# Optimization experiments

Hardware: AMD Instinct MI355X
Metric: run time of the kernel (lower is better)

## Reference

```python
import jax, jax.numpy as jnp
import numpy as np

EPS = 1e-5  # torch BatchNorm default eps


def _bn(x, gamma, beta, axes):
    # training-mode batch norm over `axes`, channel dim is axis 1
    mean = jnp.mean(x, axis=axes, keepdims=True)
    var = jnp.var(x, axis=axes, keepdims=True)
    shape = [1] * x.ndim
    shape[1] = -1
    return (x - mean) * jax.lax.rsqrt(var + EPS) * gamma.reshape(shape) + beta.reshape(shape)


def setup_inputs() -> dict:
    B, C, N = 16, 512, 192
    S_RATIO, R_RATIO = 4, 8
    Cs, Cr = C // S_RATIO, C // R_RATIO  # 128, 64
    inter = N * Cr + C  # 12800
    key = jax.random.key(0)
    ks = jax.random.split(key, 6)

    def w(k, shp, fan):
        return jax.random.normal(k, shp, jnp.float32) * np.float32(np.sqrt(2.0 / fan))

    return {
        "inputs": jax.random.normal(ks[0], (B, C, N), jnp.float32),
        "retain": 0,
        "theta_w": w(ks[1], (Cs, C), Cs), "theta_b": jnp.zeros((Cs,), jnp.float32),
        "theta_g": jnp.ones((Cs,), jnp.float32), "theta_be": jnp.zeros((Cs,), jnp.float32),
        "phi_w": w(ks[2], (Cs, C), Cs), "phi_b": jnp.zeros((Cs,), jnp.float32),
        "phi_g": jnp.ones((Cs,), jnp.float32), "phi_be": jnp.zeros((Cs,), jnp.float32),
        "re_w": w(ks[3], (Cr, Cs), Cr), "re_b": jnp.zeros((Cr,), jnp.float32),
        "re_g": jnp.ones((Cr,), jnp.float32), "re_be": jnp.zeros((Cr,), jnp.float32),
        "att_w": w(ks[4], (C, inter), C), "att_b": jnp.zeros((C,), jnp.float32),
        "att_g": jnp.ones((C,), jnp.float32), "att_be": jnp.zeros((C,), jnp.float32),
    }


def reference(inputs, retain, theta_w, theta_b, theta_g, theta_be,
              phi_w, phi_b, phi_g, phi_be, re_w, re_b, re_g, re_be,
              att_w, att_b, att_g, att_be):
    B, C, N = inputs.shape
    xt = inputs.transpose(0, 2, 1)  # [B, N, C]

    # theta / phi pro_blocks: Linear -> BN1d (over B,N) -> ReLU, output [B, Cs, N]
    th = jax.nn.relu(_bn(jnp.einsum('bnc,oc->bon', xt, theta_w) + theta_b[None, :, None], theta_g, theta_be, (0, 2)))
    ph = jax.nn.relu(_bn(jnp.einsum('bnc,oc->bon', xt, phi_w) + phi_b[None, :, None], phi_g, phi_be, (0, 2)))
    th = th.transpose(0, 2, 1)  # [B, N, Cs]
    ph = ph.transpose(0, 2, 1)  # [B, N, Cs]

    # pairwise broadcast-diff: [B, N, N, Cs]
    diff = th[:, :, None, :] - ph[:, None, :, :]

    # pro_block1: Linear -> BN2d -> ReLU, then flatten to [B, N, N*Cr]
    rel = jnp.einsum('bijc,oc->boij', diff, re_w) + re_b[None, :, None, None]  # [B, Cr, N, N]
    rel = jax.nn.relu(_bn(rel, re_g, re_be, (0, 2, 3)))
    rel = rel.transpose(0, 2, 3, 1).reshape(B, N, -1)  # [B, N, N*Cr]

    # attention_generator: Linear -> BN1d -> sigmoid, output [B, C, N]
    cat = jnp.concatenate([xt, rel], axis=2)  # [B, N, C + N*Cr]
    att = jnp.einsum('bni,oi->bon', cat, att_w) + att_b[None, :, None]  # [B, C, N]
    att = jax.nn.sigmoid(_bn(att, att_g, att_be, (0, 2)))

    features = att * inputs  # [B, C, N]
    if retain:
        return features
    return jnp.sum(features, axis=2) / jnp.sum(att, axis=2)  # [B, C]
```

## Files before the change

kernel.cpp:

```cpp
#include <hip/hip_runtime.h>

#define BB 16
#define CC 512
#define NN 192
#define CS 128
#define CR 64
#define EPSF 1e-5f
#define PART (BB*CC*NN)

typedef __attribute__((ext_vector_type(8))) short short8;
typedef __attribute__((ext_vector_type(4))) float f32x4;
typedef __attribute__((ext_vector_type(4))) unsigned int uint4v;

#define OFF_LIN2  0
#define OFF_P2    786432
#define OFF_QT    983040
#define OFF_ATTP4 1179648
#define OFF_WBF   7471104
#define OFF_XT    10747904
#define OFF_ROWS  11534336
#define OFF_SPART 11567104

__device__ __forceinline__ unsigned pkbf(float a, float b){
  unsigned r; asm("v_cvt_pk_bf16_f32 %0, %1, %2" : "=v"(r) : "v"(a), "v"(b)); return r;
}

__device__ __forceinline__ void gload_lds16(const void* g, void* l){
  __builtin_amdgcn_global_load_lds(
      (const __attribute__((address_space(1))) unsigned int*)g,
      (__attribute__((address_space(3))) unsigned int*)l, 16, 0, 0);
}

__global__ __launch_bounds__(256) void kconvxt(
    const float* __restrict__ aw, const float* __restrict__ x,
    short* __restrict__ wbf, short* __restrict__ xT)
{
  __shared__ float Ts[64][65];
  if (blockIdx.x < 3200) {
    int t = blockIdx.x*256 + threadIdx.x;
    int o2 = t / 1600;
    int kk = (t - o2*1600) * 8;
    const float* src = &aw[o2*12800 + kk];
    float4 v0 = *reinterpret_cast<const float4*>(src);
    float4 v1 = *reinterpret_cast<const float4*>(src+4);
    uint4v w;
    w.x = pkbf(v0.x, v0.y); w.y = pkbf(v0.z, v0.w);
    w.z = pkbf(v1.x, v1.y); w.w = pkbf(v1.z, v1.w);
    *reinterpret_cast<uint4v*>(&wbf[o2*12800 + kk]) = w;
  } else {
    int bid = blockIdx.x - 3200;
    int nt = bid % 3; int ct = (bid/3) & 7; int b = bid / 24;
    int c0 = ct*64, n0 = nt*64;
    int tid = threadIdx.x;
    int col = tid & 63, r0 = tid >> 6;
    #pragma unroll
    for (int it = 0; it < 16; ++it){
      int r = r0 + it*4;
      Ts[r][col] = x[(b*CC + c0 + r)*NN + n0 + col];
    }
    __syncthreads();
    #pragma unroll
    for (int it = 0; it < 2; ++it){
      int cp = it*256 + tid;
      int nr = cp >> 3, cc8 = (cp & 7)*8;
      uint4v wv;
      wv.x = pkbf(Ts[cc8+0][nr], Ts[cc8+1][nr]);
      wv.y = pkbf(Ts[cc8+2][nr], Ts[cc8+3][nr]);
      wv.z = pkbf(Ts[cc8+4][nr], Ts[cc8+5][nr]);
      wv.w = pkbf(Ts[cc8+6][nr], Ts[cc8+7][nr]);
      *reinterpret_cast<uint4v*>(&xT[((b*NN) + n0 + nr)*CC + c0 + cc8]) = wv;
    }
  }
}

__global__ __launch_bounds__(256) void k1_lin(
    const float* __restrict__ x, const float* __restrict__ wth,
    const float* __restrict__ wph, float* __restrict__ lin2,
    float* __restrict__ spart)
{
  int bid = blockIdx.x;
  int nt = bid % 3; int ch = (bid/3) & 3; int b = (bid/12) & 15; int path = bid/192;
  int cs0 = ch*32, n0 = nt*64;
  const float* w = path ? wph : wth;
  int tid = threadIdx.x;
  int ty = tid >> 4, tx = tid & 15;
  __shared__ float Xs[32][64];
  __shared__ float Ws[32][36];
  float acc[2][4];
  #pragma unroll
  for (int i=0;i<2;++i)
    #pragma unroll
    for (int j=0;j<4;++j) acc[i][j]=0.f;
  for (int c0 = 0; c0 < CC; c0 += 32){
    __syncthreads();
    {
      int nn = tid & 63, cb = tid >> 6;
      #pragma unroll
      for (int it = 0; it < 8; ++it)
        Xs[cb + it*4][nn] = x[(b*CC + c0 + cb + it*4)*NN + n0 + nn];
    }
    {
      int cc = tid & 31, sb = tid >> 5;
      #pragma unroll
      for (int it = 0; it < 4; ++it)
        Ws[cc][sb + it*8] = w[(cs0 + sb + it*8)*CC + c0 + cc];
    }
    __syncthreads();
    #pragma unroll 8
    for (int cc = 0; cc < 32; ++cc){
      float w2[2], x4[4];
      w2[0] = Ws[cc][ty*2]; w2[1] = Ws[cc][ty*2+1];
      *reinterpret_cast<float4*>(x4) = *reinterpret_cast<const float4*>(&Xs[cc][tx*4]);
      #pragma unroll
      for (int i=0;i<2;++i)
        #pragma unroll
        for (int j=0;j<4;++j) acc[i][j] += w2[i]*x4[j];
    }
  }
  #pragma unroll
  for (int r = 0; r < 2; ++r){
    int cs = cs0 + ty*2 + r;
    float4 v = make_float4(acc[r][0],acc[r][1],acc[r][2],acc[r][3]);
    *reinterpret_cast<float4*>(&lin2[(b*256 + path*128 + cs)*NN + n0 + tx*4]) = v;
  }
  #pragma unroll
  for (int r = 0; r < 2; ++r){
    float s = acc[r][0]+acc[r][1]+acc[r][2]+acc[r][3];
    float q = acc[r][0]*acc[r][0]+acc[r][1]*acc[r][1]
            + acc[r][2]*acc[r][2]+acc[r][3]*acc[r][3];
    #pragma unroll
    for (int off=8; off; off>>=1){ s += __shfl_down(s,off,16); q += __shfl_down(q,off,16); }
    if (tx==0){
      int cs2 = path*128 + cs0 + ty*2 + r;
      spart[cs2*48 + b*3 + nt] = s;
      spart[12288 + cs2*48 + b*3 + nt] = q;
    }
  }
}

__global__ __launch_bounds__(256) void k3_gemm(
    const float* __restrict__ lin2, const float* __restrict__ spart,
    const float* __restrict__ tg, const float* __restrict__ tbe,
    const float* __restrict__ pg, const float* __restrict__ pbe,
    const float* __restrict__ rw,
    float* __restrict__ p2raw, float* __restrict__ qTraw,
    float* __restrict__ rows8)
{
  int bid = blockIdx.x;
  int ih = bid & 7; int b = (bid>>3) & 15; int path = bid >> 7;
  int i0 = ih*24;
  __shared__ float Ls[128][24];
  __shared__ float Ws[64][132];
  __shared__ float sscl[512];
  int tid = threadIdx.x;
  {
    int c2 = tid;
    float s=0.f, q=0.f;
    #pragma unroll 8
    for (int i=0;i<48;++i){ s += spart[c2*48+i]; q += spart[12288+c2*48+i]; }
    float mean = s * (1.f/3072.f);
    float var = q * (1.f/3072.f) - mean*mean;
    int pth = c2 >> 7, c = c2 & 127;
    float g  = pth ? pg[c]  : tg[c];
    float be = pth ? pbe[c] : tbe[c];
    float a = g * rsqrtf(var + EPSF);
    sscl[c2] = a; sscl[256+c2] = be - mean*a;
  }
  __syncthreads();
  #pragma unroll
  for (int it = 0; it < 3; ++it){
    int cp = it*256 + tid;
    int row = cp / 6, c4 = cp - row*6;
    float a = sscl[path*128 + row], d = sscl[256 + path*128 + row];
    float4 v = *reinterpret_cast<const float4*>(&lin2[(b*256 + path*128 + row)*NN + i0 + c4*4]);
    float4 r;
    r.x = fmaxf(a*v.x + d, 0.f); r.y = fmaxf(a*v.y + d, 0.f);
    r.z = fmaxf(a*v.z + d, 0.f); r.w = fmaxf(a*v.w + d, 0.f);
    *reinterpret_cast<float4*>(&Ls[row][c4*4]) = r;
  }
  #pragma unroll
  for (int it = 0; it < 8; ++it){
    int cp = it*256 + tid;
    int o = cp >> 5, c4 = cp & 31;
    *reinterpret_cast<float4*>(&Ws[o][c4*4]) =
      *reinterpret_cast<const float4*>(&rw[o*CS + c4*4]);
  }
  __syncthreads();
  int oy = tid >> 3, ix = tid & 7;
  float acc[2][3];
  #pragma unroll
  for (int r=0;r<2;++r)
    #pragma unroll
    for (int e=0;e<3;++e) acc[r][e]=0.f;
  #pragma unroll 4
  for (int c = 0; c < 128; ++c){
    float w2[2], l3[3];
    #pragma unroll
    for (int r=0;r<2;++r) w2[r] = Ws[oy*2+r][c];
    #pragma unroll
    for (int e=0;e<3;++e) l3[e] = Ls[c][ix*3+e];
    #pragma unroll
    for (int r=0;r<2;++r)
      #pragma unroll
      for (int e=0;e<3;++e) acc[r][e] += w2[r]*l3[e];
  }
  float* dst = path ? qTraw : p2raw;
  #pragma unroll
  for (int r=0;r<2;++r)
    #pragma unroll
    for (int e=0;e<3;++e)
      dst[(b*NN + i0 + ix*3 + e)*64 + oy*2 + r] = acc[r][e];
  #pragma unroll
  for (int r=0;r<2;++r){
    float s = acc[r][0]+acc[r][1]+acc[r][2];
    float q = acc[r][0]*acc[r][0]+acc[r][1]*acc[r][1]+acc[r][2]*acc[r][2];
    #pragma unroll
    for (int off=4; off; off>>=1){ s += __shfl_down(s,off,8); q += __shfl_down(q,off,8); }
    if (ix==0){
      int o = oy*2+r;
      int ri = (path*1024 + b*64 + o)*8 + ih;
      rows8[ri] = s; rows8[16384 + ri] = q;
    }
  }
}

__global__ __launch_bounds__(256) void k5_mfma(
    const short* __restrict__ wbf, const short* __restrict__ xT,
    const float* __restrict__ p2raw, const float* __restrict__ qTraw,
    const float* __restrict__ rows8,
    const float* __restrict__ rg, const float* __restrict__ rbe,
    float* __restrict__ attp4)
{
  int bid = blockIdx.x;
  int nt = bid & 1, mt = (bid >> 1) & 3, b = (bid >> 3) & 15, ks = bid >> 7;
  int o20 = mt*128, n0 = nt*96;
  int j0 = ks*48;

  int tid = threadIdx.x;
  int w = tid >> 6, lane = tid & 63;
  int wr = w >> 1, wc = w & 1;
  int l15 = lane & 15, l4 = lane >> 4;
  int cq = tid & 7;

  __shared__ __align__(16) short As[128*64];
  __shared__ __align__(16) short Bs[96*64];
  __shared__ __align__(16) float qlds[2][64];
  __shared__ float srel[128];
  __shared__ float sred[4][5][64];

  {
    int o = tid & 63, g = tid >> 6;
    float sa=0,sb=0,saq=0,sbq=0,cross=0;
    #pragma unroll
    for (int bb=g*4; bb<g*4+4; ++bb){
      float ra=0, rb=0;
      #pragma unroll
      for (int ih=0; ih<8; ++ih){
        int ia = (bb*64+o)*8 + ih, ib = (1024 + bb*64+o)*8 + ih;
        ra += rows8[ia]; rb += rows8[ib];
        saq += rows8[16384 + ia]; sbq += rows8[16384 + ib];
      }
      sa += ra; sb += rb; cross += ra*rb;
    }
    sred[g][0][o]=sa; sred[g][1][o]=sb; sred[g][2][o]=saq;
    sred[g][3][o]=sbq; sred[g][4][o]=cross;
  }
  __syncthreads();
  if (tid < 64){
    int o = tid;
    float sa=0,sb=0,saq=0,sbq=0,cross=0;
    #pragma unroll
    for (int g=0; g<4; ++g){
      sa += sred[g][0][o]; sb += sred[g][1][o]; saq += sred[g][2][o];
      sbq += sred[g][3][o]; cross += sred[g][4][o];
    }
    float mean = (sa - sb) * (1.f/3072.f);
    float e2 = (saq + sbq) * (1.f/3072.f) - cross * (2.f/589824.f);
    float var = e2 - mean*mean;
    float s = rg[o] * rsqrtf(var + EPSF);
    srel[o] = s;
    srel[64+o] = rbe[o] - s*mean;
  }
  __syncthreads();

  float pr[3][8];
  {
    float sc8[8], sh8[8];
    #pragma unroll
    for (int k=0;k<8;++k){ sc8[k] = srel[cq*8+k]; sh8[k] = srel[64+cq*8+k]; }
    #pragma unroll
    for (int it=0; it<3; ++it){
      int n = it*32 + (tid >> 3);
      const float* pp = &p2raw[(size_t)((b*NN) + n0 + n)*64 + cq*8];
      float4 u0 = *reinterpret_cast<const float4*>(pp);
      float4 u1 = *reinterpret_cast<const float4*>(pp+4);
      pr[it][0]=sc8[0]*u0.x+sh8[0]; pr[it][1]=sc8[1]*u0.y+sh8[1];
      pr[it][2]=sc8[2]*u0.z+sh8[2]; pr[it][3]=sc8[3]*u0.w+sh8[3];
      pr[it][4]=sc8[4]*u1.x+sh8[4]; pr[it][5]=sc8[5]*u1.y+sh8[5];
      pr[it][6]=sc8[6]*u1.z+sh8[6]; pr[it][7]=sc8[7]*u1.w+sh8[7];
    }
  }
  if (tid < 64) qlds[0][tid] = srel[tid] * qTraw[(size_t)(b*NN + j0)*64 + tid];

  auto stageA = [&](int colbase){
    #pragma unroll
    for (int it=0; it<4; ++it){
      int cp = w*256 + it*64 + lane;
      int row = cp >> 3, c = (cp & 7) ^ (row & 7);
      gload_lds16(&wbf[(o20 + row)*12800 + colbase + c*8],
                  &As[(w*256 + it*64)*8]);
    }
  };
  auto stageBx = [&](int colbase){
    #pragma unroll
    for (int it=0; it<3; ++it){
      int cp = w*192 + it*64 + lane;
      int row = cp >> 3, c = (cp & 7) ^ (row & 7);
      gload_lds16(&xT[(size_t)((b*NN) + n0 + row)*CC + colbase + c*8],
                  &Bs[(w*192 + it*64)*8]);
    }
  };

  f32x4 acc[4][3];
  #pragma unroll
  for (int mi=0;mi<4;++mi)
    #pragma unroll
    for (int ni=0;ni<3;++ni) acc[mi][ni] = (f32x4){0.f,0.f,0.f,0.f};

  auto mfma_phase = [&](){
    #pragma unroll
    for (int s=0; s<2; ++s){
      short8 av[4], bv[3];
      int c = s*4 + l4;
      #pragma unroll
      for (int mi=0; mi<4; ++mi){
        int row = wr*64 + mi*16 + l15;
        av[mi] = *reinterpret_cast<const short8*>(&As[row*64 + ((c ^ (row&7))<<3)]);
      }
      #pragma unroll
      for (int ni=0; ni<3; ++ni){
        int rown = wc*48 + ni*16 + l15;
        bv[ni] = *reinterpret_cast<const short8*>(&Bs[rown*64 + ((c ^ (rown&7))<<3)]);
      }
      #pragma unroll
      for (int mi=0; mi<4; ++mi)
        #pragma unroll
        for (int ni=0; ni<3; ++ni)
          acc[mi][ni] = __builtin_amdgcn_mfma_f32_16x16x32_bf16(av[mi], bv[ni], acc[mi][ni], 0, 0, 0);
    }
  };

  #pragma unroll
  for (int kt = 0; kt < 2; ++kt){
    __syncthreads();
    stageA(ks*128 + kt*64);
    stageBx(ks*128 + kt*64);
    __syncthreads();
    mfma_phase();
  }

  for (int kt = 0; kt < 48; ++kt){
    __syncthreads();
    stageA(512 + (j0 + kt)*64);
    if (tid < 64 && kt < 47)
      qlds[(kt+1)&1][tid] = srel[tid] * qTraw[(size_t)(b*NN + j0 + kt + 1)*64 + tid];
    {
      const float* qq = qlds[kt&1];
      float4 qa = *reinterpret_cast<const float4*>(&qq[cq*8]);
      float4 qb = *reinterpret_cast<const float4*>(&qq[cq*8+4]);
      #pragma unroll
      for (int it=0; it<3; ++it){
        float r0 = fmaxf(pr[it][0]-qa.x, 0.f);
        float r1 = fmaxf(pr[it][1]-qa.y, 0.f);
        float r2 = fmaxf(pr[it][2]-qa.z, 0.f);
        float r3 = fmaxf(pr[it][3]-qa.w, 0.f);
        float r4 = fmaxf(pr[it][4]-qb.x, 0.f);
        float r5 = fmaxf(pr[it][5]-qb.y, 0.f);
        float r6 = fmaxf(pr[it][6]-qb.z, 0.f);
        float r7 = fmaxf(pr[it][7]-qb.w, 0.f);
        uint4v wv;
        wv.x = pkbf(r0,r1); wv.y = pkbf(r2,r3);
        wv.z = pkbf(r4,r5); wv.w = pkbf(r6,r7);
        int n = it*32 + (tid >> 3);
        *reinterpret_cast<uint4v*>(&Bs[n*64 + ((cq ^ (n&7))<<3)]) = wv;
      }
    }
    __syncthreads();
    mfma_phase();
  }

  float* dst = attp4 + (size_t)ks*PART;
  #pragma unroll
  for (int mi=0; mi<4; ++mi){
    #pragma unroll
    for (int r=0; r<4; ++r){
      int o2 = o20 + wr*64 + mi*16 + l4*4 + r;
      #pragma unroll
      for (int ni=0; ni<3; ++ni){
        int n = n0 + wc*48 + ni*16 + l15;
        dst[(b*CC + o2)*NN + n] = acc[mi][ni][r];
      }
    }
  }
}

__global__ __launch_bounds__(256) void k67(
    const float* __restrict__ p4, const float* __restrict__ x,
    const float* __restrict__ g, const float* __restrict__ be,
    float* __restrict__ out)
{
  int o2 = blockIdx.x;
  int tid = threadIdx.x;
  int b = tid >> 4, nl = tid & 15;
  float v[12], xv[12];
  float s=0.f, q=0.f;
  #pragma unroll
  for (int it=0; it<6; ++it){
    int n = nl*2 + it*32;
    int idx = (b*CC + o2)*NN + n;
    float t0=0.f, t1=0.f;
    #pragma unroll
    for (int p=0; p<4; ++p){
      float2 u = *reinterpret_cast<const float2*>(&p4[(size_t)p*PART + idx]);
      t0 += u.x; t1 += u.y;
    }
    float2 xu = *reinterpret_cast<const float2*>(&x[idx]);
    v[it*2] = t0; v[it*2+1] = t1;
    xv[it*2] = xu.x; xv[it*2+1] = xu.y;
    s += t0 + t1; q += t0*t0 + t1*t1;
  }
  __shared__ float rs[4], rq[4], ad[2];
  #pragma unroll
  for (int off=32; off; off>>=1){ s += __shfl_down(s,off); q += __shfl_down(q,off); }
  int w = tid >> 6;
  if ((tid & 63)==0){ rs[w]=s; rq[w]=q; }
  __syncthreads();
  if (tid==0){
    s = rs[0]+rs[1]+rs[2]+rs[3]; q = rq[0]+rq[1]+rq[2]+rq[3];
    float mean = s * (1.f/3072.f);
    float var = q * (1.f/3072.f) - mean*mean;
    float a = g[o2] * rsqrtf(var + EPSF);
    ad[0] = a; ad[1] = be[o2] - mean*a;
  }
  __syncthreads();
  float a = ad[0], d = ad[1];
  float sf=0.f, ss=0.f;
  #pragma unroll
  for (int it=0; it<12; ++it){
    float sig = 1.f/(1.f + expf(-(a*v[it] + d)));
    sf += sig * xv[it]; ss += sig;
  }
  #pragma unroll
  for (int off=8; off; off>>=1){ sf += __shfl_down(sf,off,16); ss += __shfl_down(ss,off,16); }
  if (nl==0) out[b*CC + o2] = sf/ss;
}

extern "C" void kernel_launch(void* const* d_in, const int* in_sizes, int n_in,
                              void* d_out, int out_size, void* d_ws, size_t ws_size,
                              hipStream_t stream)
{
  const float* inputs  = (const float*)d_in[0];
  const float* theta_w = (const float*)d_in[2];
  const float* theta_g = (const float*)d_in[4];
  const float* theta_be= (const float*)d_in[5];
  const float* phi_w   = (const float*)d_in[6];
  const float* phi_g   = (const float*)d_in[8];
  const float* phi_be  = (const float*)d_in[9];
  const float* re_w    = (const float*)d_in[10];
  const float* re_g    = (const float*)d_in[12];
  const float* re_be   = (const float*)d_in[13];
  const float* att_w   = (const float*)d_in[14];
  const float* att_g   = (const float*)d_in[16];
  const float* att_be  = (const float*)d_in[17];

  float* ws = (float*)d_ws;
  float* lin2  = ws + OFF_LIN2;
  float* p2raw = ws + OFF_P2;
  float* qTraw = ws + OFF_QT;
  float* attp4 = ws + OFF_ATTP4;
  short* wbf   = (short*)(ws + OFF_WBF);
  short* xT    = (short*)(ws + OFF_XT);
  float* rows8 = ws + OFF_ROWS;
  float* spart = ws + OFF_SPART;

  kconvxt<<<3584, 256, 0, stream>>>(att_w, inputs, wbf, xT);
  k1_lin<<<384, 256, 0, stream>>>(inputs, theta_w, phi_w, lin2, spart);
  k3_gemm<<<256, 256, 0, stream>>>(lin2, spart, theta_g, theta_be, phi_g, phi_be,
                                   re_w, p2raw, qTraw, rows8);
  k5_mfma<<<512, 256, 0, stream>>>(wbf, xT, p2raw, qTraw, rows8, re_g, re_be, attp4);
  k67<<<512, 256, 0, stream>>>(attp4, inputs, att_g, att_be, (float*)d_out);
}
```

Baseline: 128.4 us.

## Double-buffer weight tiles and preload all q rows into LDS in k5_mfma

The A (weight) tile in LDS is now double-buffered, so the global-to-LDS load for the next j-step is issued before the current step's MFMAs and waited on with a partial vmcnt instead of a full barrier. All 48 q rows for the block are prefetched into LDS once and scaled up front, replacing the per-iteration global q load. MFMA phases also raise wave priority with s_setprio. This costs extra LDS (a second 16KB A buffer plus 12KB for q), which may lower occupancy, and the hand-written waitcnt counts depend on exactly how many loads are outstanding.

```diff
diff --git a/kernel.cpp b/kernel.cpp
--- a/kernel.cpp
+++ b/kernel.cpp
@@ -242,9 +242,9 @@
   int l15 = lane & 15, l4 = lane >> 4;
   int cq = tid & 7;
 
-  __shared__ __align__(16) short As[128*64];
+  __shared__ __align__(16) short As[2][128*64];
   __shared__ __align__(16) short Bs[96*64];
-  __shared__ __align__(16) float qlds[2][64];
+  __shared__ __align__(16) float qall[48*64];
   __shared__ float srel[128];
   __shared__ float sred[4][5][64];
 
@@ -264,6 +264,14 @@
     }
     sred[g][0][o]=sa; sred[g][1][o]=sb; sred[g][2][o]=saq;
     sred[g][3][o]=sbq; sred[g][4][o]=cross;
+  }
+  {
+    const float* qsrc = &qTraw[(size_t)(b*NN + j0)*64];
+    #pragma unroll
+    for (int it=0; it<3; ++it){
+      int cp = it*256 + tid;
+      gload_lds16(qsrc + cp*4, &qall[cp*4]);
+    }
   }
   __syncthreads();
   if (tid < 64){
@@ -300,15 +308,14 @@
       pr[it][6]=sc8[6]*u1.z+sh8[6]; pr[it][7]=sc8[7]*u1.w+sh8[7];
     }
   }
-  if (tid < 64) qlds[0][tid] = srel[tid] * qTraw[(size_t)(b*NN + j0)*64 + tid];
-
-  auto stageA = [&](int colbase){
+
+  auto stageA = [&](int buf, int colbase){
     #pragma unroll
     for (int it=0; it<4; ++it){
       int cp = w*256 + it*64 + lane;
       int row = cp >> 3, c = (cp & 7) ^ (row & 7);
       gload_lds16(&wbf[(o20 + row)*12800 + colbase + c*8],
-                  &As[(w*256 + it*64)*8]);
+                  &As[buf][(w*256 + it*64)*8]);
     }
   };
   auto stageBx = [&](int colbase){
@@ -327,7 +334,8 @@
     #pragma unroll
     for (int ni=0;ni<3;++ni) acc[mi][ni] = (f32x4){0.f,0.f,0.f,0.f};
 
-  auto mfma_phase = [&](){
+  auto mfma_phase = [&](int buf){
+    __builtin_amdgcn_s_setprio(1);
     #pragma unroll
     for (int s=0; s<2; ++s){
       short8 av[4], bv[3];
@@ -335,7 +343,7 @@
       #pragma unroll
       for (int mi=0; mi<4; ++mi){
         int row = wr*64 + mi*16 + l15;
-        av[mi] = *reinterpret_cast<const short8*>(&As[row*64 + ((c ^ (row&7))<<3)]);
+        av[mi] = *reinterpret_cast<const short8*>(&As[buf][row*64 + ((c ^ (row&7))<<3)]);
       }
       #pragma unroll
       for (int ni=0; ni<3; ++ni){
@@ -348,24 +356,32 @@
         for (int ni=0; ni<3; ++ni)
           acc[mi][ni] = __builtin_amdgcn_mfma_f32_16x16x32_bf16(av[mi], bv[ni], acc[mi][ni], 0, 0, 0);
     }
+    __builtin_amdgcn_s_setprio(0);
   };
 
   #pragma unroll
   for (int kt = 0; kt < 2; ++kt){
     __syncthreads();
-    stageA(ks*128 + kt*64);
+    stageA(0, ks*128 + kt*64);
     stageBx(ks*128 + kt*64);
+    if (kt == 0){
+      #pragma unroll
+      for (int it=0; it<12; ++it){
+        int i = it*256 + tid;
+        qall[i] *= srel[i & 63];
+      }
+    }
     __syncthreads();
-    mfma_phase();
-  }
-
+    mfma_phase(0);
+  }
+
+  __syncthreads();
+  stageA(0, 512 + j0*64);
   for (int kt = 0; kt < 48; ++kt){
-    __syncthreads();
-    stageA(512 + (j0 + kt)*64);
-    if (tid < 64 && kt < 47)
-      qlds[(kt+1)&1][tid] = srel[tid] * qTraw[(size_t)(b*NN + j0 + kt + 1)*64 + tid];
+    int cur = kt & 1;
+    if (kt < 47) stageA(cur^1, 512 + (j0 + kt + 1)*64);
     {
-      const float* qq = qlds[kt&1];
+      const float* qq = &qall[kt*64];
       float4 qa = *reinterpret_cast<const float4*>(&qq[cq*8]);
       float4 qb = *reinterpret_cast<const float4*>(&qq[cq*8+4]);
       #pragma unroll
@@ -385,8 +401,12 @@
         *reinterpret_cast<uint4v*>(&Bs[n*64 + ((cq ^ (n&7))<<3)]) = wv;
       }
     }
-    __syncthreads();
-    mfma_phase();
+    if (kt < 47) asm volatile("s_waitcnt vmcnt(4) lgkmcnt(0)" ::: "memory");
+    else         asm volatile("s_waitcnt vmcnt(0) lgkmcnt(0)" ::: "memory");
+    __builtin_amdgcn_sched_barrier(0);
+    __builtin_amdgcn_s_barrier();
+    mfma_phase(cur);
+    __builtin_amdgcn_s_barrier();
   }
 
   float* dst = attp4 + (size_t)ks*PART;
```

Result: faster. 118.7 us (-7.5%).
